# Optimization experiments

Hardware: AMD Instinct MI355X
Metric: run time of the kernel (lower is better)

Reference implementation:

```python
import jax, jax.numpy as jnp
import numpy as np

LAMBDA_INIT = 0.8


def setup_inputs() -> dict:
    key = jax.random.key(0)
    ks = jax.random.split(key, 12)
    B, T, E = 2, 2048, 1024
    H = 8            # num_heads // 2 diff-heads
    HS = 64          # head_size
    DO = 128         # 2 * head_output_dimension (per-head output dim)
    q = jax.random.normal(ks[0], (B, T, E), jnp.float32)
    k = jax.random.normal(ks[1], (B, T, E), jnp.float32)
    v = jax.random.normal(ks[2], (B, T, E), jnp.float32)
    s = E ** -0.5  # linear-layer style init scale
    Wq = jax.random.normal(ks[3], (H, E, 2 * HS), jnp.float32) * s
    Wk = jax.random.normal(ks[4], (H, E, 2 * HS), jnp.float32) * s
    Wv = jax.random.normal(ks[5], (H, E, DO), jnp.float32) * s
    # lambda reparam vectors (scaled 0.1 to keep exp(dot) numerically tame)
    lq1 = jax.random.normal(ks[6], (H, HS), jnp.float32) * 0.1
    lk1 = jax.random.normal(ks[7], (H, HS), jnp.float32) * 0.1
    lq2 = jax.random.normal(ks[8], (H, HS), jnp.float32) * 0.1
    lk2 = jax.random.normal(ks[9], (H, HS), jnp.float32) * 0.1
    Wp = jax.random.normal(ks[10], (H * DO, E), jnp.float32) * (H * DO) ** -0.5
    bp = jnp.zeros((E,), jnp.float32)
    # buffer: tril(ones, diagonal=1); positions where it is 0 get -inf
    mask = jnp.tril(jnp.ones((T, T), jnp.bool_), 1)
    return {"q": q, "k": k, "v": v, "Wq": Wq, "Wk": Wk, "Wv": Wv,
            "lq1": lq1, "lk1": lk1, "lq2": lq2, "lk2": lk2,
            "Wp": Wp, "bp": bp, "mask": mask}


def reference(q, k, v, Wq, Wk, Wv, lq1, lk1, lq2, lk2, Wp, bp, mask):
    B, T, E = q.shape
    H = Wq.shape[0]
    HS = Wq.shape[-1] // 2
    scale = HS ** -0.5
    Q = jnp.einsum('bte,hed->bhtd', q, Wq)   # [B,H,T,2HS]
    K = jnp.einsum('bte,hed->bhtd', k, Wk)
    V = jnp.einsum('bte,hed->bhtd', v, Wv)   # [B,H,T,DO]
    Q1, Q2 = jnp.split(Q, 2, axis=-1)
    K1, K2 = jnp.split(K, 2, axis=-1)
    neg_inf = jnp.float32(-jnp.inf)
    s1 = jnp.einsum('bhtd,bhsd->bhts', Q1, K1) * scale
    s2 = jnp.einsum('bhtd,bhsd->bhts', Q2, K2) * scale
    s1 = jnp.where(mask[:T, :T], s1, neg_inf)
    s2 = jnp.where(mask[:T, :T], s2, neg_inf)
    a1 = jax.nn.softmax(s1, axis=-1)
    a2 = jax.nn.softmax(s2, axis=-1)
    lbd = (jnp.exp(jnp.sum(lq1 * lk1, -1)) - jnp.exp(jnp.sum(lq2 * lk2, -1))
           + LAMBDA_INIT)                     # [H]
    attn = a1 - lbd[None, :, None, None] * a2
    ctx = jnp.einsum('bhts,bhsd->bhtd', attn, V) * (1.0 - LAMBDA_INIT)
    out = ctx.transpose(0, 2, 1, 3).reshape(B, T, -1)  # concat heads
    return out @ Wp + bp
```

## Files before the change

kernel.cpp:

```cpp
#include <hip/hip_runtime.h>
#include <hip/hip_bf16.h>


constexpr int Tn = 2048;
constexpr int En = 1024;
constexpr int Hn = 8;
constexpr float LAMBDA_INIT = 0.8f;
constexpr float QSCALE = 0.18033688011112042f;
constexpr size_t SZb = (size_t)2 * Tn * En;
constexpr size_t WSZ = (size_t)En * En;

typedef __attribute__((ext_vector_type(8))) short short8;
typedef __attribute__((ext_vector_type(4))) short s16x4;
typedef __attribute__((ext_vector_type(4))) float f32x4;

__device__ __forceinline__ short f2bf(float x) {
  union { __hip_bfloat16 h; short s; } u;
  u.h = __float2bfloat16(x);
  return u.s;
}
__device__ __forceinline__ void gload16(const short* g, short* l) {
  __builtin_amdgcn_global_load_lds(
      (const __attribute__((address_space(1))) void*)g,
      (__attribute__((address_space(3))) void*)l, 16, 0, 0);
}

__global__ __launch_bounds__(256)
void prep(const float* __restrict__ q, const float* __restrict__ k,
          const float* __restrict__ v,
          const float* __restrict__ Wq, const float* __restrict__ Wk,
          const float* __restrict__ Wv, const float* __restrict__ Wp,
          short* __restrict__ ws, short* __restrict__ WT) {
  __shared__ float tl[64][65];
  const int id = blockIdx.x;
  const int tid = threadIdx.x;
  if (id < 6144) {
    const int by = id >> 11;
    const int bx = id & 2047;
    const float* src = (by == 0) ? q : (by == 1) ? k : v;
    short* dst = ws + (size_t)by * SZb;
    const size_t i = ((size_t)bx * 256 + tid) * 8;
    float4 a = *(const float4*)&src[i];
    float4 b = *(const float4*)&src[i + 4];
    short8 o;
    o[0] = f2bf(a.x); o[1] = f2bf(a.y); o[2] = f2bf(a.z); o[3] = f2bf(a.w);
    o[4] = f2bf(b.x); o[5] = f2bf(b.y); o[6] = f2bf(b.z); o[7] = f2bf(b.w);
    *(short8*)&dst[i] = o;
    return;
  }
  const int wid = id - 6144;
  const float* src;
  short* dst;
  int r0, c0, C;
  if (wid < 768) {
    const int wi = wid >> 8;
    const float* W = (wi == 0) ? Wq : (wi == 1) ? Wk : Wv;
    const int rem = wid & 255;
    const int h = rem >> 5;
    const int tile = rem & 31;
    r0 = (tile >> 1) * 64;
    c0 = (tile & 1) * 64;
    C = 128;
    src = W + (size_t)h * En * 128;
    dst = WT + (size_t)wi * WSZ + (size_t)h * 128 * En;
  } else {
    const int idx = wid - 768;
    r0 = (idx >> 4) * 64;
    c0 = (idx & 15) * 64;
    C = En;
    src = Wp;
    dst = WT + 3 * WSZ;
  }
  const int r = tid >> 2, cc = (tid & 3) * 16;
#pragma unroll
  for (int j = 0; j < 4; ++j) {
    const float4 x = *(const float4*)&src[(size_t)(r0 + r) * C + c0 + cc + j * 4];
    tl[r][cc + j * 4 + 0] = x.x;
    tl[r][cc + j * 4 + 1] = x.y;
    tl[r][cc + j * 4 + 2] = x.z;
    tl[r][cc + j * 4 + 3] = x.w;
  }
  __syncthreads();
  const int c = tid >> 2, rc = (tid & 3) * 16;
  short8 o0, o1;
#pragma unroll
  for (int e = 0; e < 8; ++e) {
    o0[e] = f2bf(tl[rc + e][c]);
    o1[e] = f2bf(tl[rc + 8 + e][c]);
  }
  *(short8*)&dst[(size_t)(c0 + c) * En + r0 + rc] = o0;
  *(short8*)&dst[(size_t)(c0 + c) * En + r0 + rc + 8] = o1;
}

__global__ __launch_bounds__(256)
void qkv_mfma2(const short* __restrict__ Xq, const short* __restrict__ Xk,
               const short* __restrict__ Xv, const short* __restrict__ WT,
               short* __restrict__ Qo, short* __restrict__ Ko,
               short* __restrict__ Vto) {
  __shared__ __align__(16) short As[2][4096];
  __shared__ __align__(16) short Bs2[2][4096];
  const int which = blockIdx.z;
  const short* X = (which == 0) ? Xq : (which == 1) ? Xk : Xv;
  const int head = blockIdx.y;
  const int m0 = blockIdx.x * 128;
  const short* Bt = WT + (size_t)which * WSZ + (size_t)head * 128 * En;
  const float oscale = (which == 0) ? QSCALE : 1.0f;

  const int tid = threadIdx.x;
  const int lane = tid & 63;
  const int w = tid >> 6, wr = w >> 1, wc = w & 1;
  const int fr = lane & 15, fk = (lane >> 4) * 8;
  const int srow = tid >> 2, sch = (tid & 3) * 8;
  const int wdst = w * 512;

#define QSTAGE(BUF, K0)                                                  \
  {                                                                      \
    _Pragma("unroll") for (int j = 0; j < 2; ++j) {                      \
      gload16(&X[(size_t)(m0 + j * 64 + srow) * En + (K0) + sch],        \
              &As[BUF][j * 2048 + wdst]);                                \
      gload16(&Bt[(size_t)(j * 64 + srow) * En + (K0) + sch],            \
              &Bs2[BUF][j * 2048 + wdst]);                               \
    }                                                                    \
  }

  f32x4 acc[4][4] = {};
  QSTAGE(0, 0);
  for (int k0 = 0; k0 < En; k0 += 32) {
    const int cur = (k0 >> 5) & 1;
    if (k0 + 32 < En) {
      QSTAGE(cur ^ 1, k0 + 32);
      __builtin_amdgcn_sched_barrier(0);
      asm volatile("s_waitcnt vmcnt(4)" ::: "memory");
      __builtin_amdgcn_sched_barrier(0);
    } else {
      __builtin_amdgcn_sched_barrier(0);
      asm volatile("s_waitcnt vmcnt(0)" ::: "memory");
      __builtin_amdgcn_sched_barrier(0);
    }
    __builtin_amdgcn_s_barrier();

    short8 a[4], b[4];
#pragma unroll
    for (int i = 0; i < 4; ++i)
      a[i] = *(const short8*)&As[cur][(wr * 64 + i * 16 + fr) * 32 + fk];
#pragma unroll
    for (int j = 0; j < 4; ++j)
      b[j] = *(const short8*)&Bs2[cur][(wc * 64 + j * 16 + fr) * 32 + fk];
#pragma unroll
    for (int i = 0; i < 4; ++i)
#pragma unroll
      for (int j = 0; j < 4; ++j)
        acc[i][j] = __builtin_amdgcn_mfma_f32_16x16x32_bf16(a[i], b[j],
                                                            acc[i][j], 0, 0, 0);
    __builtin_amdgcn_s_barrier();
  }
#undef QSTAGE

  const int crow = (lane >> 4) * 4, ccol = lane & 15;
  if (which == 2) {
#pragma unroll
    for (int i = 0; i < 4; ++i) {
      const int m = m0 + wr * 64 + i * 16 + crow;
      const int bb = m >> 11, t = m & (Tn - 1);
#pragma unroll
      for (int j = 0; j < 4; ++j) {
        const int d = wc * 64 + j * 16 + ccol;
        s16x4 pk;
#pragma unroll
        for (int p = 0; p < 4; ++p) pk[p] = f2bf(acc[i][j][p]);
        *(s16x4*)&Vto[((size_t)(bb * Hn + head) * 128 + d) * Tn + t] = pk;
      }
    }
  } else {
    short* Out = (which == 0) ? Qo : Ko;
#pragma unroll
    for (int i = 0; i < 4; ++i) {
      const int m = m0 + wr * 64 + i * 16 + crow;
      const int bb = m >> 11, t = m & (Tn - 1);
      short* dst = Out + ((size_t)(bb * Hn + head) * Tn + t) * 128;
#pragma unroll
      for (int j = 0; j < 4; ++j) {
        const int d = wc * 64 + j * 16 + ccol;
#pragma unroll
        for (int p = 0; p < 4; ++p)
          dst[(size_t)p * 128 + d] = f2bf(acc[i][j][p] * oscale);
      }
    }
  }
}

__global__ __launch_bounds__(256)
void proj_mfma2(const short* __restrict__ Xb, const short* __restrict__ WpT,
                const float* __restrict__ bias, float* __restrict__ Out) {
  __shared__ __align__(16) short As[2][2048];
  __shared__ __align__(16) short Bs2[2][4096];
  const int m0 = blockIdx.x * 64;
  const int n0 = blockIdx.y * 128;

  const int tid = threadIdx.x;
  const int lane = tid & 63;
  const int w = tid >> 6, wr = w >> 1, wc = w & 1;
  const int fr = lane & 15, fk = (lane >> 4) * 8;
  const int srow = tid >> 2, sch = (tid & 3) * 8;
  const int wdst = w * 512;

#define PSTAGE(BUF, K0)                                                  \
  {                                                                      \
    gload16(&Xb[(size_t)(m0 + srow) * En + (K0) + sch],                  \
            &As[BUF][wdst]);                                             \
    _Pragma("unroll") for (int j = 0; j < 2; ++j)                        \
      gload16(&WpT[(size_t)(n0 + j * 64 + srow) * En + (K0) + sch],      \
              &Bs2[BUF][j * 2048 + wdst]);                               \
  }

  f32x4 acc[2][4] = {};
  PSTAGE(0, 0);
  for (int k0 = 0; k0 < En; k0 += 32) {
    const int cur = (k0 >> 5) & 1;
    if (k0 + 32 < En) {
      PSTAGE(cur ^ 1, k0 + 32);
      __builtin_amdgcn_sched_barrier(0);
      asm volatile("s_waitcnt vmcnt(3)" ::: "memory");
      __builtin_amdgcn_sched_barrier(0);
    } else {
      __builtin_amdgcn_sched_barrier(0);
      asm volatile("s_waitcnt vmcnt(0)" ::: "memory");
      __builtin_amdgcn_sched_barrier(0);
    }
    __builtin_amdgcn_s_barrier();

    short8 a[2], b[4];
#pragma unroll
    for (int i = 0; i < 2; ++i)
      a[i] = *(const short8*)&As[cur][(wr * 32 + i * 16 + fr) * 32 + fk];
#pragma unroll
    for (int j = 0; j < 4; ++j)
      b[j] = *(const short8*)&Bs2[cur][(wc * 64 + j * 16 + fr) * 32 + fk];
#pragma unroll
    for (int i = 0; i < 2; ++i)
#pragma unroll
      for (int j = 0; j < 4; ++j)
        acc[i][j] = __builtin_amdgcn_mfma_f32_16x16x32_bf16(a[i], b[j],
                                                            acc[i][j], 0, 0, 0);
    __builtin_amdgcn_s_barrier();
  }
#undef PSTAGE

  const int crow = (lane >> 4) * 4, ccol = lane & 15;
#pragma unroll
  for (int i = 0; i < 2; ++i) {
    const int m = m0 + wr * 32 + i * 16 + crow;
#pragma unroll
    for (int j = 0; j < 4; ++j) {
      const int n = n0 + wc * 64 + j * 16 + ccol;
      const float bv = bias[n];
#pragma unroll
      for (int p = 0; p < 4; ++p)
        Out[(size_t)(m + p) * En + n] = acc[i][j][p] + bv;
    }
  }
}

__global__ __launch_bounds__(256, 4)
void diff_attn11(const short* __restrict__ Qg, const short* __restrict__ Kg,
                 const short* __restrict__ Vtg,
                 const float* __restrict__ lq1, const float* __restrict__ lk1,
                 const float* __restrict__ lq2, const float* __restrict__ lk2,
                 short* __restrict__ ctxb) {
  __shared__ __align__(16) short pool[18688];

  const int lin = blockIdx.x;
  const int h = lin & 7;
  const int idx = lin >> 3;
  const int b = idx >> 5;
  const int x = idx & 31;
  const int tid = threadIdx.x;
  const int lane = tid & 63;
  const int w = tid >> 6;
  const int st = w >> 1, wh = w & 1;
  const int fr = lane & 15, hi = lane >> 4;
  const int swz = fr & 7;
  const int swv = (fr ^ (fr >> 2)) & 3;
  const size_t basebh = (size_t)(b * Hn + h) * Tn * 128;

  float lbd;
  {
    float a1 = lq1[h * 64 + lane] * lk1[h * 64 + lane];
    float a2 = lq2[h * 64 + lane] * lk2[h * 64 + lane];
#pragma unroll
    for (int off = 1; off <= 32; off <<= 1) {
      a1 += __shfl_xor(a1, off);
      a2 += __shfl_xor(a2, off);
    }
    lbd = __expf(a1) - __expf(a2) + LAMBDA_INIT;
  }

  int ksrc[2], vsrc[2], dsto[2];
#pragma unroll
  for (int j = 0; j < 2; ++j) {
    const int ob = j * 4096 + tid * 16;
    { const int s = ob >> 8, cp = (ob >> 4) & 15, c = cp ^ (s & 7);
      ksrc[j] = s * 128 + c * 8; }
    { const int d = ob >> 6, cp = (ob >> 4) & 3,
          c = cp ^ ((d ^ (d >> 2)) & 3);
      vsrc[j] = d * Tn + c * 8; }
    dsto[j] = (j * 4096 + w * 1024) >> 1;
  }
  const short* kgb = Kg + basebh;
  const short* vgb = Vtg + basebh;

#define STAGE(BUF, S0)                                                   \
  {                                                                      \
    const short* kb_ = kgb + (size_t)(S0) * 128;                         \
    const short* vb_ = vgb + (S0);                                       \
    _Pragma("unroll") for (int j = 0; j < 2; ++j) {                      \
      gload16(kb_ + ksrc[j], pool + (BUF) * 4096 + dsto[j]);             \
      gload16(vb_ + vsrc[j], pool + 8192 + (BUF) * 4096 + dsto[j]);      \
    }                                                                    \
  }

  short8 ones;
#pragma unroll
  for (int e = 0; e < 8; ++e) ones[e] = (short)0x3F80;
  short* Plw = pool + 16384 + w * 576;

  auto phase = [&](int qi) {
    const int q0 = qi * 32;
    const int NT = min(Tn / 32, qi + 2);
    const int tmin = q0 + wh * 16;
    const int tbase = tmin + hi * 4;

    short8 qf[2];
    {
      const short* qp = Qg + basebh + (size_t)(tmin + fr) * 128 + st * 64;
      qf[0] = *(const short8*)(qp + hi * 8);
      qf[1] = *(const short8*)(qp + 32 + hi * 8);
    }
    f32x4 o[8] = {};
    f32x4 ol = {};

    STAGE(0, 0);
    __builtin_amdgcn_sched_barrier(0);
    asm volatile("s_waitcnt vmcnt(0)" ::: "memory");
    __builtin_amdgcn_sched_barrier(0);
    __builtin_amdgcn_s_barrier();

    int cur = 0;
    for (int t = 0; t < NT; ++t) {
      const int s0 = t * 32;
      if (t + 1 < NT) STAGE(cur ^ 1, s0 + 32);

      if (s0 <= tmin + 16) {
        const short* Kb = pool + cur * 4096;
        const short* Vb = pool + 8192 + cur * 4096;
        const bool interior = (tmin - s0) >= 30;

        f32x4 s4[2] = {};
        __builtin_amdgcn_s_setprio(1);
#pragma unroll
        for (int sb = 0; sb < 2; ++sb) {
          const int rb = (sb * 16 + fr) * 128;
#pragma unroll
          for (int kp = 0; kp < 2; ++kp) {
            const short8 kb = *(const short8*)
                &Kb[rb + ((st * 8 + ((kp * 4 + hi) ^ swz)) << 3)];
            s4[sb] = __builtin_amdgcn_mfma_f32_16x16x32_bf16(qf[kp], kb,
                                                             s4[sb], 0, 0, 0);
          }
        }
        __builtin_amdgcn_s_setprio(0);
        if (!interior) {
#pragma unroll
          for (int sb = 0; sb < 2; ++sb) {
            const int sg = s0 + sb * 16 + fr;
#pragma unroll
            for (int p = 0; p < 4; ++p)
              if (sg > tbase + p + 1) s4[sb][p] = -1e30f;
          }
        }

#pragma unroll
        for (int sb = 0; sb < 2; ++sb)
#pragma unroll
          for (int p = 0; p < 4; ++p)
            Plw[(hi * 4 + p) * 36 + sb * 16 + fr] =
                f2bf(exp2f(s4[sb][p] - 12.0f));

        const short8 pf = *(const short8*)&Plw[fr * 36 + hi * 8];
        __builtin_amdgcn_s_setprio(1);
        ol = __builtin_amdgcn_mfma_f32_16x16x32_bf16(ones, pf, ol, 0, 0, 0);
#pragma unroll
        for (int dblk = 0; dblk < 8; ++dblk) {
          const short8 va = *(const short8*)
              &Vb[(dblk * 16 + fr) * 32 + ((hi ^ swv) << 3)];
          o[dblk] = __builtin_amdgcn_mfma_f32_16x16x32_bf16(va, pf, o[dblk],
                                                            0, 0, 0);
        }
        __builtin_amdgcn_s_setprio(0);
      }

      __builtin_amdgcn_sched_barrier(0);
      asm volatile("s_waitcnt vmcnt(0)" ::: "memory");
      __builtin_amdgcn_sched_barrier(0);
      __builtin_amdgcn_s_barrier();
      cur ^= 1;
    }

    const float lr = ol[0];
    float* O2L = (float*)pool;
    if (st == 1) {
      const float c2 = (1.0f - LAMBDA_INIT) * lbd / lr;
#pragma unroll
      for (int dblk = 0; dblk < 8; ++dblk)
#pragma unroll
        for (int e = 0; e < 4; ++e)
          O2L[wh * 2176 + (dblk * 16 + hi * 4 + e) * 17 + fr] =
              c2 * o[dblk][e];
    }
    __syncthreads();
    if (st == 0) {
      const float c1 = (1.0f - LAMBDA_INIT) / lr;
      const int t = tmin + fr;
      short* dst = ctxb + ((size_t)b * Tn + t) * En + h * 128;
#pragma unroll
      for (int dblk = 0; dblk < 8; ++dblk) {
        s16x4 pk;
#pragma unroll
        for (int e = 0; e < 4; ++e)
          pk[e] = f2bf(c1 * o[dblk][e] -
                       O2L[wh * 2176 + (dblk * 16 + hi * 4 + e) * 17 + fr]);
        *(s16x4*)&dst[dblk * 16 + hi * 4] = pk;
      }
    }
    __syncthreads();
  };

  phase(63 - x);
  phase(x);
#undef STAGE
}

extern "C" void kernel_launch(void* const* d_in, const int* in_sizes, int n_in,
                              void* d_out, int out_size, void* d_ws, size_t ws_size,
                              hipStream_t stream) {
  const float* q   = (const float*)d_in[0];
  const float* k   = (const float*)d_in[1];
  const float* v   = (const float*)d_in[2];
  const float* Wq  = (const float*)d_in[3];
  const float* Wk  = (const float*)d_in[4];
  const float* Wv  = (const float*)d_in[5];
  const float* lq1 = (const float*)d_in[6];
  const float* lk1 = (const float*)d_in[7];
  const float* lq2 = (const float*)d_in[8];
  const float* lk2 = (const float*)d_in[9];
  const float* Wp  = (const float*)d_in[10];
  const float* bp  = (const float*)d_in[11];

  short* ws = (short*)d_ws;
  short* qbf = ws;
  short* kbf = ws + SZb;
  short* vbf = ws + 2 * SZb;
  short* Qb  = ws + 3 * SZb;
  short* Kb  = ws + 4 * SZb;
  short* Vtb = ws + 5 * SZb;
  short* WT  = ws + 6 * SZb;
  short* ctxb = qbf;

  prep<<<dim3(7168), dim3(256), 0, stream>>>(q, k, v, Wq, Wk, Wv, Wp,
                                             ws, WT);
  qkv_mfma2<<<dim3(32, 8, 3), dim3(256), 0, stream>>>(qbf, kbf, vbf, WT,
                                                      Qb, Kb, Vtb);
  diff_attn11<<<dim3(512), dim3(256), 0, stream>>>(Qb, Kb, Vtb,
                                                   lq1, lk1, lq2, lk2, ctxb);
  proj_mfma2<<<dim3(64, 8), dim3(256), 0, stream>>>(ctxb, WT + 3 * WSZ, bp,
                                                    (float*)d_out);
}
```

Before: 142.9 us.

## Fuse fp32-to-bf16 activation conversion into QKV projection GEMM A-tile loads

```diff
diff --git a/kernel.cpp b/kernel.cpp
--- a/kernel.cpp
+++ b/kernel.cpp
@@ -26,29 +26,12 @@
 }
 
 __global__ __launch_bounds__(256)
-void prep(const float* __restrict__ q, const float* __restrict__ k,
-          const float* __restrict__ v,
-          const float* __restrict__ Wq, const float* __restrict__ Wk,
+void prep(const float* __restrict__ Wq, const float* __restrict__ Wk,
           const float* __restrict__ Wv, const float* __restrict__ Wp,
-          short* __restrict__ ws, short* __restrict__ WT) {
+          short* __restrict__ WT) {
   __shared__ float tl[64][65];
-  const int id = blockIdx.x;
+  const int wid = blockIdx.x;
   const int tid = threadIdx.x;
-  if (id < 6144) {
-    const int by = id >> 11;
-    const int bx = id & 2047;
-    const float* src = (by == 0) ? q : (by == 1) ? k : v;
-    short* dst = ws + (size_t)by * SZb;
-    const size_t i = ((size_t)bx * 256 + tid) * 8;
-    float4 a = *(const float4*)&src[i];
-    float4 b = *(const float4*)&src[i + 4];
-    short8 o;
-    o[0] = f2bf(a.x); o[1] = f2bf(a.y); o[2] = f2bf(a.z); o[3] = f2bf(a.w);
-    o[4] = f2bf(b.x); o[5] = f2bf(b.y); o[6] = f2bf(b.z); o[7] = f2bf(b.w);
-    *(short8*)&dst[i] = o;
-    return;
-  }
-  const int wid = id - 6144;
   const float* src;
   short* dst;
   int r0, c0, C;
@@ -93,14 +76,14 @@
 }
 
 __global__ __launch_bounds__(256)
-void qkv_mfma2(const short* __restrict__ Xq, const short* __restrict__ Xk,
-               const short* __restrict__ Xv, const short* __restrict__ WT,
+void qkv_mfma3(const float* __restrict__ q, const float* __restrict__ k,
+               const float* __restrict__ v, const short* __restrict__ WT,
                short* __restrict__ Qo, short* __restrict__ Ko,
                short* __restrict__ Vto) {
   __shared__ __align__(16) short As[2][4096];
   __shared__ __align__(16) short Bs2[2][4096];
   const int which = blockIdx.z;
-  const short* X = (which == 0) ? Xq : (which == 1) ? Xk : Xv;
+  const float* X = (which == 0) ? q : (which == 1) ? k : v;
   const int head = blockIdx.y;
   const int m0 = blockIdx.x * 128;
   const short* Bt = WT + (size_t)which * WSZ + (size_t)head * 128 * En;
@@ -110,34 +93,51 @@
   const int lane = tid & 63;
   const int w = tid >> 6, wr = w >> 1, wc = w & 1;
   const int fr = lane & 15, fk = (lane >> 4) * 8;
+  const int arow = tid >> 1, ah = (tid & 1) * 16;
   const int srow = tid >> 2, sch = (tid & 3) * 8;
   const int wdst = w * 512;
 
-#define QSTAGE(BUF, K0)                                                  \
-  {                                                                      \
-    _Pragma("unroll") for (int j = 0; j < 2; ++j) {                      \
-      gload16(&X[(size_t)(m0 + j * 64 + srow) * En + (K0) + sch],        \
-              &As[BUF][j * 2048 + wdst]);                                \
-      gload16(&Bt[(size_t)(j * 64 + srow) * En + (K0) + sch],            \
-              &Bs2[BUF][j * 2048 + wdst]);                               \
-    }                                                                    \
-  }
+  float4 xa[4];
+  auto AQLOAD = [&](int k0) {
+#pragma unroll
+    for (int qq = 0; qq < 4; ++qq)
+      xa[qq] = *(const float4*)&X[(size_t)(m0 + arow) * En + k0 + ah + qq * 4];
+  };
+  auto ACVT = [&](int buf) {
+    short8 p0, p1;
+#pragma unroll
+    for (int e = 0; e < 4; ++e) {
+      p0[e]     = f2bf(((const float*)&xa[0])[e]);
+      p0[e + 4] = f2bf(((const float*)&xa[1])[e]);
+      p1[e]     = f2bf(((const float*)&xa[2])[e]);
+      p1[e + 4] = f2bf(((const float*)&xa[3])[e]);
+    }
+    *(short8*)&As[buf][arow * 32 + ah] = p0;
+    *(short8*)&As[buf][arow * 32 + ah + 8] = p1;
+  };
+  auto BSTAGE = [&](int buf, int k0) {
+#pragma unroll
+    for (int j = 0; j < 2; ++j)
+      gload16(&Bt[(size_t)(j * 64 + srow) * En + k0 + sch],
+              &Bs2[buf][j * 2048 + wdst]);
+  };
 
   f32x4 acc[4][4] = {};
-  QSTAGE(0, 0);
+  AQLOAD(0);
+  BSTAGE(0, 0);
+  ACVT(0);
+  __builtin_amdgcn_sched_barrier(0);
+  asm volatile("s_waitcnt vmcnt(0) lgkmcnt(0)" ::: "memory");
+  __builtin_amdgcn_sched_barrier(0);
+  __builtin_amdgcn_s_barrier();
+
   for (int k0 = 0; k0 < En; k0 += 32) {
     const int cur = (k0 >> 5) & 1;
-    if (k0 + 32 < En) {
-      QSTAGE(cur ^ 1, k0 + 32);
-      __builtin_amdgcn_sched_barrier(0);
-      asm volatile("s_waitcnt vmcnt(4)" ::: "memory");
-      __builtin_amdgcn_sched_barrier(0);
-    } else {
-      __builtin_amdgcn_sched_barrier(0);
-      asm volatile("s_waitcnt vmcnt(0)" ::: "memory");
-      __builtin_amdgcn_sched_barrier(0);
-    }
-    __builtin_amdgcn_s_barrier();
+    const bool more = (k0 + 32 < En);
+    if (more) {
+      AQLOAD(k0 + 32);
+      BSTAGE(cur ^ 1, k0 + 32);
+    }
 
     short8 a[4], b[4];
 #pragma unroll
@@ -152,9 +152,14 @@
       for (int j = 0; j < 4; ++j)
         acc[i][j] = __builtin_amdgcn_mfma_f32_16x16x32_bf16(a[i], b[j],
                                                             acc[i][j], 0, 0, 0);
+
+    if (more) ACVT(cur ^ 1);
+
+    __builtin_amdgcn_sched_barrier(0);
+    asm volatile("s_waitcnt vmcnt(0) lgkmcnt(0)" ::: "memory");
+    __builtin_amdgcn_sched_barrier(0);
     __builtin_amdgcn_s_barrier();
   }
-#undef QSTAGE
 
   const int crow = (lane >> 4) * 4, ccol = lane & 15;
   if (which == 2) {
@@ -457,18 +462,14 @@
   const float* bp  = (const float*)d_in[11];
 
   short* ws = (short*)d_ws;
-  short* qbf = ws;
-  short* kbf = ws + SZb;
-  short* vbf = ws + 2 * SZb;
-  short* Qb  = ws + 3 * SZb;
-  short* Kb  = ws + 4 * SZb;
-  short* Vtb = ws + 5 * SZb;
-  short* WT  = ws + 6 * SZb;
-  short* ctxb = qbf;
-
-  prep<<<dim3(7168), dim3(256), 0, stream>>>(q, k, v, Wq, Wk, Wv, Wp,
-                                             ws, WT);
-  qkv_mfma2<<<dim3(32, 8, 3), dim3(256), 0, stream>>>(qbf, kbf, vbf, WT,
+  short* Qb   = ws;
+  short* Kb   = ws + SZb;
+  short* Vtb  = ws + 2 * SZb;
+  short* WT   = ws + 3 * SZb;
+  short* ctxb = ws + 4 * SZb;
+
+  prep<<<dim3(1024), dim3(256), 0, stream>>>(Wq, Wk, Wv, Wp, WT);
+  qkv_mfma3<<<dim3(32, 8, 3), dim3(256), 0, stream>>>(q, k, v, WT,
                                                       Qb, Kb, Vtb);
   diff_attn11<<<dim3(512), dim3(256), 0, stream>>>(Qb, Kb, Vtb,
                                                    lq1, lk1, lq2, lk2, ctxb);
```

After: 163.2 us. 14.2% more time.

## Software-pipeline QK^T one tile ahead with triple-buffered K staging

Applied to the files above, without the earlier changes.

```diff
diff --git a/kernel.cpp b/kernel.cpp
--- a/kernel.cpp
+++ b/kernel.cpp
@@ -261,13 +261,13 @@
   }
 }
 
-__global__ __launch_bounds__(256, 4)
-void diff_attn11(const short* __restrict__ Qg, const short* __restrict__ Kg,
+__global__ __launch_bounds__(256, 2)
+void diff_attn13(const short* __restrict__ Qg, const short* __restrict__ Kg,
                  const short* __restrict__ Vtg,
                  const float* __restrict__ lq1, const float* __restrict__ lk1,
                  const float* __restrict__ lq2, const float* __restrict__ lk2,
                  short* __restrict__ ctxb) {
-  __shared__ __align__(16) short pool[18688];
+  __shared__ __align__(16) short pool[22784];
 
   const int lin = blockIdx.x;
   const int h = lin & 7;
@@ -309,20 +309,23 @@
   const short* kgb = Kg + basebh;
   const short* vgb = Vtg + basebh;
 
-#define STAGE(BUF, S0)                                                   \
+#define STAGE_K(BUF, S0)                                                 \
   {                                                                      \
     const short* kb_ = kgb + (size_t)(S0) * 128;                         \
+    _Pragma("unroll") for (int j = 0; j < 2; ++j)                        \
+      gload16(kb_ + ksrc[j], pool + (BUF) * 4096 + dsto[j]);             \
+  }
+#define STAGE_V(BUF, S0)                                                 \
+  {                                                                      \
     const short* vb_ = vgb + (S0);                                       \
-    _Pragma("unroll") for (int j = 0; j < 2; ++j) {                      \
-      gload16(kb_ + ksrc[j], pool + (BUF) * 4096 + dsto[j]);             \
-      gload16(vb_ + vsrc[j], pool + 8192 + (BUF) * 4096 + dsto[j]);      \
-    }                                                                    \
+    _Pragma("unroll") for (int j = 0; j < 2; ++j)                        \
+      gload16(vb_ + vsrc[j], pool + 12288 + (BUF) * 4096 + dsto[j]);     \
   }
 
   short8 ones;
 #pragma unroll
   for (int e = 0; e < 8; ++e) ones[e] = (short)0x3F80;
-  short* Plw = pool + 16384 + w * 576;
+  short* Plw = pool + 20480 + w * 576;
 
   auto phase = [&](int qi) {
     const int q0 = qi * 32;
@@ -339,36 +342,46 @@
     f32x4 o[8] = {};
     f32x4 ol = {};
 
-    STAGE(0, 0);
+    auto qk = [&](int tt, f32x4(&s)[2]) {
+      const short* Kb = pool + (tt % 3) * 4096;
+      __builtin_amdgcn_s_setprio(1);
+#pragma unroll
+      for (int sb = 0; sb < 2; ++sb) {
+        const int rb = (sb * 16 + fr) * 128;
+#pragma unroll
+        for (int kp = 0; kp < 2; ++kp) {
+          const short8 kb = *(const short8*)
+              &Kb[rb + ((st * 8 + ((kp * 4 + hi) ^ swz)) << 3)];
+          s[sb] = __builtin_amdgcn_mfma_f32_16x16x32_bf16(qf[kp], kb,
+                                                          s[sb], 0, 0, 0);
+        }
+      }
+      __builtin_amdgcn_s_setprio(0);
+    };
+
+    STAGE_K(0, 0);
+    STAGE_V(0, 0);
+    STAGE_K(1, 32);
     __builtin_amdgcn_sched_barrier(0);
     asm volatile("s_waitcnt vmcnt(0)" ::: "memory");
     __builtin_amdgcn_sched_barrier(0);
     __builtin_amdgcn_s_barrier();
 
-    int cur = 0;
+    f32x4 s4[2] = {};
+    qk(0, s4);
+
     for (int t = 0; t < NT; ++t) {
       const int s0 = t * 32;
-      if (t + 1 < NT) STAGE(cur ^ 1, s0 + 32);
+      if (t + 2 < NT) STAGE_K((t + 2) % 3, (t + 2) * 32);
+      if (t + 1 < NT) STAGE_V((t + 1) & 1, (t + 1) * 32);
+
+      f32x4 s4n[2] = {};
+      const bool nact = (t + 1 < NT) && ((t + 1) * 32 <= tmin + 16);
+      if (nact) qk(t + 1, s4n);
 
       if (s0 <= tmin + 16) {
-        const short* Kb = pool + cur * 4096;
-        const short* Vb = pool + 8192 + cur * 4096;
+        const short* Vb = pool + 12288 + (t & 1) * 4096;
         const bool interior = (tmin - s0) >= 30;
-
-        f32x4 s4[2] = {};
-        __builtin_amdgcn_s_setprio(1);
-#pragma unroll
-        for (int sb = 0; sb < 2; ++sb) {
-          const int rb = (sb * 16 + fr) * 128;
-#pragma unroll
-          for (int kp = 0; kp < 2; ++kp) {
-            const short8 kb = *(const short8*)
-                &Kb[rb + ((st * 8 + ((kp * 4 + hi) ^ swz)) << 3)];
-            s4[sb] = __builtin_amdgcn_mfma_f32_16x16x32_bf16(qf[kp], kb,
-                                                             s4[sb], 0, 0, 0);
-          }
-        }
-        __builtin_amdgcn_s_setprio(0);
         if (!interior) {
 #pragma unroll
           for (int sb = 0; sb < 2; ++sb) {
@@ -399,11 +412,13 @@
         __builtin_amdgcn_s_setprio(0);
       }
 
+      s4[0] = s4n[0];
+      s4[1] = s4n[1];
+
       __builtin_amdgcn_sched_barrier(0);
       asm volatile("s_waitcnt vmcnt(0)" ::: "memory");
       __builtin_amdgcn_sched_barrier(0);
       __builtin_amdgcn_s_barrier();
-      cur ^= 1;
     }
 
     const float lr = ol[0];
@@ -437,7 +452,8 @@
 
   phase(63 - x);
   phase(x);
-#undef STAGE
+#undef STAGE_K
+#undef STAGE_V
 }
 
 extern "C" void kernel_launch(void* const* d_in, const int* in_sizes, int n_in,
@@ -470,7 +486,7 @@
                                              ws, WT);
   qkv_mfma2<<<dim3(32, 8, 3), dim3(256), 0, stream>>>(qbf, kbf, vbf, WT,
                                                       Qb, Kb, Vtb);
-  diff_attn11<<<dim3(512), dim3(256), 0, stream>>>(Qb, Kb, Vtb,
+  diff_attn13<<<dim3(512), dim3(256), 0, stream>>>(Qb, Kb, Vtb,
                                                    lq1, lk1, lq2, lk2, ctxb);
   proj_mfma2<<<dim3(64, 8), dim3(256), 0, stream>>>(ctxb, WT + 3 * WSZ, bp,
                                                     (float*)d_out);
```

Result: slower. 147.7 us (+3.3%).
